# Optimization experiments

Hardware: AMD Instinct MI355X
Metric: run time of the kernel (lower is better)

The kernel has to match this reference:

```python
import jax, jax.numpy as jnp
import numpy as np

HIDDEN = 768
NUM_HEADS = 12
HEAD_DIM = HIDDEN // NUM_HEADS  # 64


def setup_inputs() -> dict:
    key = jax.random.key(0)
    ks = jax.random.split(key, 7)
    B, S = 2, 4096
    scale = 1.0 / np.sqrt(HIDDEN)
    return {
        "hidden_states": jax.random.normal(ks[0], (B, S, HIDDEN), dtype=jnp.float32),
        "Wq": jax.random.normal(ks[1], (HIDDEN, HIDDEN), dtype=jnp.float32) * scale,
        "bq": jnp.zeros((HIDDEN,), dtype=jnp.float32),
        "Wk": jax.random.normal(ks[2], (HIDDEN, HIDDEN), dtype=jnp.float32) * scale,
        "bk": jnp.zeros((HIDDEN,), dtype=jnp.float32),
        "Wv": jax.random.normal(ks[3], (HIDDEN, HIDDEN), dtype=jnp.float32) * scale,
        "bv": jnp.zeros((HIDDEN,), dtype=jnp.float32),
    }


def _split_heads(x):
    # [B, S, H] -> [B, heads, S, head_dim]
    B, S, _ = x.shape
    return x.reshape(B, S, NUM_HEADS, HEAD_DIM).transpose(0, 2, 1, 3)


def reference(hidden_states, Wq, bq, Wk, bk, Wv, bv):
    q = _split_heads(hidden_states @ Wq + bq)  # [B, h, S, d]
    k = _split_heads(hidden_states @ Wk + bk)
    v = _split_heads(hidden_states @ Wv + bv)
    scores = jnp.einsum("bhqd,bhkd->bhqk", q, k) / np.sqrt(HEAD_DIM)
    probs = jax.nn.softmax(scores, axis=-1)  # [B, h, S, S] materialized (eager attn)
    ctx = jnp.einsum("bhqk,bhkd->bhqd", probs, v)
    B, _, S, _ = ctx.shape
    return ctx.transpose(0, 2, 1, 3).reshape(B, S, HIDDEN)
```

## Files before the change

kernel.cpp:

```cpp
#include <hip/hip_runtime.h>
#include <hip/hip_bf16.h>

typedef unsigned short ushort_t;
typedef __attribute__((ext_vector_type(4))) float f32x4;
typedef __attribute__((ext_vector_type(8))) __bf16 bfrag;

#define MFMA16(a,b,c) __builtin_amdgcn_mfma_f32_16x16x32_bf16((a),(b),(c),0,0,0)

#define HID 768
#define NH 12
#define SEQ 4096
#define QSCALE 0.18033688011112042f

#define WAIT_VMCNT0() asm volatile("s_waitcnt vmcnt(0)" ::: "memory")

__device__ __forceinline__ unsigned short f2bf(float x) {
  union { float f; unsigned u; } v; v.f = x;
  unsigned r = v.u + 0x7fffu + ((v.u >> 16) & 1u);
  return (unsigned short)(r >> 16);
}

typedef const unsigned char __attribute__((address_space(1)))* gas1_t;
typedef unsigned char __attribute__((address_space(3)))* las3_t;
__device__ __forceinline__ void gload_lds16(const void* g, void* l) {
  __builtin_amdgcn_global_load_lds((gas1_t)(unsigned long long)g,
                                   (las3_t)(unsigned)(unsigned long long)l,
                                   16, 0, 0);
}

__device__ __forceinline__ f32x4 zero4() { f32x4 z = {0.f, 0.f, 0.f, 0.f}; return z; }

__global__ __launch_bounds__(256) void cvt_hidden(const float* __restrict__ hs,
                                                  ushort_t* __restrict__ A) {
  int i = blockIdx.x * 256 + threadIdx.x;
  float4 v = ((const float4*)hs)[i];
  ushort4 o;
  o.x = f2bf(v.x); o.y = f2bf(v.y); o.z = f2bf(v.z); o.w = f2bf(v.w);
  ((ushort4*)A)[i] = o;
}

__global__ __launch_bounds__(256) void transpose_w(const float* __restrict__ Wq,
                                                   const float* __restrict__ Wk,
                                                   const float* __restrict__ Wv,
                                                   ushort_t* __restrict__ Wt) {
  const int z = blockIdx.z;
  const float* W = (z == 0) ? Wq : ((z == 1) ? Wk : Wv);
  const int k0 = blockIdx.x * 64, n0 = blockIdx.y * 64;
  __shared__ float tile[64][65];
  const int t = threadIdx.x;
  const int c4 = (t & 15) * 4;
  const int r = t >> 4;
#pragma unroll
  for (int it = 0; it < 4; ++it) {
    int rr = r + it * 16;
    float4 v = *(const float4*)&W[(size_t)(k0 + rr) * HID + n0 + c4];
    tile[c4 + 0][rr] = v.x; tile[c4 + 1][rr] = v.y;
    tile[c4 + 2][rr] = v.z; tile[c4 + 3][rr] = v.w;
  }
  __syncthreads();
#pragma unroll
  for (int it = 0; it < 4; ++it) {
    int nl = r + it * 16;
    ushort4 o;
    o.x = f2bf(tile[nl][c4 + 0]); o.y = f2bf(tile[nl][c4 + 1]);
    o.z = f2bf(tile[nl][c4 + 2]); o.w = f2bf(tile[nl][c4 + 3]);
    *(ushort4*)&Wt[((size_t)z * HID + n0 + nl) * HID + k0 + c4] = o;
  }
}

__global__ __launch_bounds__(256) void qkv_gemm(const ushort_t* __restrict__ A,
                                                const ushort_t* __restrict__ Wt,
                                                const float* __restrict__ bq,
                                                const float* __restrict__ bk,
                                                const float* __restrict__ bv,
                                                ushort_t* __restrict__ Qh,
                                                ushort_t* __restrict__ Kh,
                                                ushort_t* __restrict__ Vt) {
  __shared__ ushort_t Als[128 * 64];
  __shared__ ushort_t Bls[128 * 64];
  const int z = blockIdx.z;
  const int m0 = blockIdx.x * 128, n0 = blockIdx.y * 128;
  const ushort_t* Wz = Wt + (size_t)z * HID * HID;
  const float* bias = (z == 0) ? bq : ((z == 1) ? bk : bv);
  const int t = threadIdx.x, w = t >> 6, lane = t & 63;
  const int g = lane >> 4, qc = lane & 15;
  const int srow = lane >> 3, sch = lane & 7;
  const int wm = w >> 1, wn = w & 1;

  f32x4 acc[4][4];
#pragma unroll
  for (int mt = 0; mt < 4; ++mt)
#pragma unroll
    for (int nt = 0; nt < 4; ++nt) acc[mt][nt] = zero4();

  for (int kt = 0; kt < 12; ++kt) {
    const int k0 = kt * 64;
#pragma unroll
    for (int i = 0; i < 4; ++i) {
      int row = w * 32 + i * 8 + srow;
      int chA = sch ^ (srow & 7);
      gload_lds16(&A[(size_t)(m0 + row) * HID + k0 + chA * 8],
                  &Als[(w * 32 + i * 8) * 64]);
      gload_lds16(&Wz[(size_t)(n0 + row) * HID + k0 + chA * 8],
                  &Bls[(w * 32 + i * 8) * 64]);
    }
    WAIT_VMCNT0();
    __syncthreads();
#pragma unroll
    for (int kk = 0; kk < 2; ++kk) {
      bfrag af[4], bf_[4];
#pragma unroll
      for (int mt = 0; mt < 4; ++mt) {
        int row = wm * 64 + mt * 16 + qc;
        af[mt] = *(const bfrag*)((const char*)Als + row * 128 +
                                 (((kk * 4 + g) ^ (qc & 7)) << 4));
      }
#pragma unroll
      for (int nt = 0; nt < 4; ++nt) {
        int row = wn * 64 + nt * 16 + qc;
        bf_[nt] = *(const bfrag*)((const char*)Bls + row * 128 +
                                  (((kk * 4 + g) ^ (qc & 7)) << 4));
      }
#pragma unroll
      for (int mt = 0; mt < 4; ++mt)
#pragma unroll
        for (int nt = 0; nt < 4; ++nt)
          acc[mt][nt] = MFMA16(af[mt], bf_[nt], acc[mt][nt]);
    }
    __syncthreads();
  }

#pragma unroll
  for (int mt = 0; mt < 4; ++mt) {
#pragma unroll
    for (int nt = 0; nt < 4; ++nt) {
      int n = n0 + wn * 64 + nt * 16 + qc;
      int head = n >> 6, d = n & 63;
      float bb = bias[n];
      int mB = m0 + wm * 64 + mt * 16 + 4 * g;
      int bidx = mB >> 12, s0 = mB & 4095;
      f32x4 a = acc[mt][nt];
      if (z == 2) {
        ushort4 o;
        o.x = f2bf(a[0] + bb); o.y = f2bf(a[1] + bb);
        o.z = f2bf(a[2] + bb); o.w = f2bf(a[3] + bb);
        int scol = (s0 & ~31) | (((s0 >> 2) & 3) << 3) | (((s0 >> 4) & 1) << 2);
        *(ushort4*)&Vt[((size_t)((bidx * NH + head) * 64 + d)) * SEQ + scol] = o;
      } else {
        ushort_t* dst = (z == 0) ? Qh : Kh;
        float sc = (z == 0) ? QSCALE : 1.0f;
        size_t base = (size_t)(bidx * NH + head) * SEQ;
#pragma unroll
        for (int i = 0; i < 4; ++i)
          dst[(base + s0 + i) * 64 + d] = f2bf((a[i] + bb) * sc);
      }
    }
  }
}

__device__ __forceinline__ void stage_tile(const ushort_t* __restrict__ Kb,
                                           const ushort_t* __restrict__ Vb,
                                           ushort_t* Kd, ushort_t* Vd,
                                           int kb, const int* jr, const int* jc, int w) {
#pragma unroll
  for (int i = 0; i < 2; ++i) {
    gload_lds16(&Kb[(size_t)(kb + jr[i]) * 64 + jc[i] * 8], &Kd[(w * 128 + i * 64) * 8]);
    gload_lds16(&Vb[(size_t)jr[i] * SEQ + kb + jc[i] * 8], &Vd[(w * 128 + i * 64) * 8]);
  }
}

__device__ __forceinline__ void tile_compute(const ushort_t* Kc, const ushort_t* Vc,
                                             const bfrag (&qv)[2][2],
                                             f32x4 (&o)[2][4], f32x4 (&lacc)[2],
                                             bfrag ones, int g, int qc) {
  bfrag ak[4][2];
#pragma unroll
  for (int s = 0; s < 4; ++s) {
    const int r = s * 16 + qc;
    ak[s][0] = *(const bfrag*)&Kc[r * 64 + ((g ^ (qc & 7)) * 8)];
    ak[s][1] = *(const bfrag*)&Kc[r * 64 + (((4 + g) ^ (qc & 7)) * 8)];
  }
  f32x4 st0[4], st1[4];
#pragma unroll
  for (int s = 0; s < 4; ++s) {
    f32x4 z = zero4();
    z = MFMA16(ak[s][0], qv[0][0], z);
    st0[s] = MFMA16(ak[s][1], qv[0][1], z);
  }
#pragma unroll
  for (int s = 0; s < 4; ++s) {
    f32x4 z = zero4();
    z = MFMA16(ak[s][0], qv[1][0], z);
    st1[s] = MFMA16(ak[s][1], qv[1][1], z);
  }
  bfrag bp0[2], bp1[2];
#pragma unroll
  for (int i = 0; i < 4; ++i) {
    bp0[0][i]     = (__bf16)__builtin_amdgcn_exp2f(st0[0][i]);
    bp0[0][4 + i] = (__bf16)__builtin_amdgcn_exp2f(st0[1][i]);
    bp0[1][i]     = (__bf16)__builtin_amdgcn_exp2f(st0[2][i]);
    bp0[1][4 + i] = (__bf16)__builtin_amdgcn_exp2f(st0[3][i]);
  }
  lacc[0] = MFMA16(ones, bp0[0], lacc[0]);
  lacc[0] = MFMA16(ones, bp0[1], lacc[0]);
#pragma unroll
  for (int i = 0; i < 4; ++i) {
    bp1[0][i]     = (__bf16)__builtin_amdgcn_exp2f(st1[0][i]);
    bp1[0][4 + i] = (__bf16)__builtin_amdgcn_exp2f(st1[1][i]);
    bp1[1][i]     = (__bf16)__builtin_amdgcn_exp2f(st1[2][i]);
    bp1[1][4 + i] = (__bf16)__builtin_amdgcn_exp2f(st1[3][i]);
  }
  lacc[1] = MFMA16(ones, bp1[0], lacc[1]);
  lacc[1] = MFMA16(ones, bp1[1], lacc[1]);
#pragma unroll
  for (int kk = 0; kk < 2; ++kk) {
#pragma unroll
    for (int dt = 0; dt < 4; ++dt) {
      bfrag av = *(const bfrag*)&Vc[(dt * 16 + qc) * 64 + (((kk * 4 + g) ^ (qc & 7)) * 8)];
      o[0][dt] = MFMA16(av, bp0[kk], o[0][dt]);
      o[1][dt] = MFMA16(av, bp1[kk], o[1][dt]);
    }
  }
}

__global__ __launch_bounds__(256, 3) void attn_kernel(const ushort_t* __restrict__ Qh,
                                                      const ushort_t* __restrict__ Kh,
                                                      const ushort_t* __restrict__ Vt,
                                                      float* __restrict__ out) {
  const int bh = blockIdx.y;
  const int b = bh / NH, head = bh - b * NH;
  const int t = threadIdx.x, w = t >> 6, lane = t & 63;
  const int g = lane >> 4, qc = lane & 15;
  const ushort_t* Qb = Qh + (size_t)bh * SEQ * 64;
  const ushort_t* Kb = Kh + (size_t)bh * SEQ * 64;
  const ushort_t* Vb = Vt + (size_t)bh * 64 * SEQ;
  const int q0 = blockIdx.x * 128 + w * 32;

  __shared__ ushort_t Kls[2][4096];
  __shared__ ushort_t Vls[2][4096];

  int jr[2], jc[2];
#pragma unroll
  for (int i = 0; i < 2; ++i) {
    int j = w * 128 + i * 64 + lane;
    jr[i] = j >> 3;
    jc[i] = (j & 7) ^ (jr[i] & 7);
  }

  bfrag qv[2][2];
#pragma unroll
  for (int qf = 0; qf < 2; ++qf)
#pragma unroll
    for (int dd = 0; dd < 2; ++dd)
      qv[qf][dd] = *(const bfrag*)&Qb[(size_t)(q0 + qf * 16 + qc) * 64 + dd * 32 + g * 8];

  f32x4 o[2][4];
  f32x4 lacc[2];
#pragma unroll
  for (int qf = 0; qf < 2; ++qf) {
    lacc[qf] = zero4();
#pragma unroll
    for (int dt = 0; dt < 4; ++dt) o[qf][dt] = zero4();
  }
  bfrag ones;
#pragma unroll
  for (int j = 0; j < 8; ++j) ones[j] = (__bf16)1.0f;

  stage_tile(Kb, Vb, &Kls[0][0], &Vls[0][0], 0, jr, jc, w);

  for (int kt2 = 0; kt2 < 32; ++kt2) {
    const int k0 = kt2 * 2;
    WAIT_VMCNT0();
    __syncthreads();
    stage_tile(Kb, Vb, &Kls[1][0], &Vls[1][0], (k0 + 1) * 64, jr, jc, w);
    tile_compute(&Kls[0][0], &Vls[0][0], qv, o, lacc, ones, g, qc);
    WAIT_VMCNT0();
    __syncthreads();
    if (kt2 < 31)
      stage_tile(Kb, Vb, &Kls[0][0], &Vls[0][0], (k0 + 2) * 64, jr, jc, w);
    tile_compute(&Kls[1][0], &Vls[1][0], qv, o, lacc, ones, g, qc);
  }

#pragma unroll
  for (int qf = 0; qf < 2; ++qf) {
    float inv = 1.0f / lacc[qf][0];
    int qrow = q0 + qf * 16 + qc;
    float* orow = out + (size_t)(b * SEQ + qrow) * HID + head * 64;
#pragma unroll
    for (int dt = 0; dt < 4; ++dt) {
      float4 vv;
      vv.x = o[qf][dt][0] * inv; vv.y = o[qf][dt][1] * inv;
      vv.z = o[qf][dt][2] * inv; vv.w = o[qf][dt][3] * inv;
      *(float4*)(orow + dt * 16 + 4 * g) = vv;
    }
  }
}

extern "C" void kernel_launch(void* const* d_in, const int* in_sizes, int n_in,
                              void* d_out, int out_size, void* d_ws, size_t ws_size,
                              hipStream_t stream) {
  (void)in_sizes; (void)n_in; (void)out_size; (void)ws_size;
  const float* hs = (const float*)d_in[0];
  const float* Wq = (const float*)d_in[1];
  const float* bq = (const float*)d_in[2];
  const float* Wk = (const float*)d_in[3];
  const float* bk = (const float*)d_in[4];
  const float* Wv = (const float*)d_in[5];
  const float* bv = (const float*)d_in[6];
  float* out = (float*)d_out;

  char* ws = (char*)d_ws;
  ushort_t* Abf = (ushort_t*)ws;
  ushort_t* Wt  = (ushort_t*)(ws + 12582912);
  ushort_t* Qh  = (ushort_t*)(ws + 12582912 + 3538944);
  ushort_t* Kh  = Qh + 6291456;
  ushort_t* Vt  = Kh + 6291456;

  cvt_hidden<<<6144, 256, 0, stream>>>(hs, Abf);
  transpose_w<<<dim3(12, 12, 3), 256, 0, stream>>>(Wq, Wk, Wv, Wt);
  qkv_gemm<<<dim3(64, 6, 3), 256, 0, stream>>>(Abf, Wt, bq, bk, bv, Qh, Kh, Vt);
  attn_kernel<<<dim3(32, 24), 256, 0, stream>>>(Qh, Kh, Vt, out);
}
```

Before: 165.2 us.

## Software-pipeline QK of next tile with softmax/PV of current, triple-buffer LDS

Splits the per-tile attention compute into a QK score stage and a softmax-plus-PV stage. The QK product for tile k+1 is issued alongside the exp and PV work for tile k, so MFMA and exp/VALU work can interleave. K/V LDS buffering goes from double to triple, with a loop unrolled by three and a tail PV step. This is meant to hide MFMA and exp latency within a wave. In exchange it keeps two sets of score registers live and uses 48KB of LDS per block, which may cost occupancy at 3 blocks per CU or cause spills.

```diff
diff --git a/kernel.cpp b/kernel.cpp
--- a/kernel.cpp
+++ b/kernel.cpp
@@ -13,6 +13,7 @@
 #define QSCALE 0.18033688011112042f
 
 #define WAIT_VMCNT0() asm volatile("s_waitcnt vmcnt(0)" ::: "memory")
+#define WAIT_VMCNT4() asm volatile("s_waitcnt vmcnt(4)" ::: "memory")
 
 __device__ __forceinline__ unsigned short f2bf(float x) {
   union { float f; unsigned u; } v; v.f = x;
@@ -169,10 +170,8 @@
   }
 }
 
-__device__ __forceinline__ void tile_compute(const ushort_t* Kc, const ushort_t* Vc,
-                                             const bfrag (&qv)[2][2],
-                                             f32x4 (&o)[2][4], f32x4 (&lacc)[2],
-                                             bfrag ones, int g, int qc) {
+__device__ __forceinline__ void qk_tile(const ushort_t* Kc, const bfrag (&qv)[2][2],
+                                        f32x4 (&st)[2][4], int g, int qc) {
   bfrag ak[4][2];
 #pragma unroll
   for (int s = 0; s < 4; ++s) {
@@ -180,47 +179,40 @@
     ak[s][0] = *(const bfrag*)&Kc[r * 64 + ((g ^ (qc & 7)) * 8)];
     ak[s][1] = *(const bfrag*)&Kc[r * 64 + (((4 + g) ^ (qc & 7)) * 8)];
   }
-  f32x4 st0[4], st1[4];
-#pragma unroll
-  for (int s = 0; s < 4; ++s) {
-    f32x4 z = zero4();
-    z = MFMA16(ak[s][0], qv[0][0], z);
-    st0[s] = MFMA16(ak[s][1], qv[0][1], z);
-  }
-#pragma unroll
-  for (int s = 0; s < 4; ++s) {
-    f32x4 z = zero4();
-    z = MFMA16(ak[s][0], qv[1][0], z);
-    st1[s] = MFMA16(ak[s][1], qv[1][1], z);
-  }
-  bfrag bp0[2], bp1[2];
-#pragma unroll
-  for (int i = 0; i < 4; ++i) {
-    bp0[0][i]     = (__bf16)__builtin_amdgcn_exp2f(st0[0][i]);
-    bp0[0][4 + i] = (__bf16)__builtin_amdgcn_exp2f(st0[1][i]);
-    bp0[1][i]     = (__bf16)__builtin_amdgcn_exp2f(st0[2][i]);
-    bp0[1][4 + i] = (__bf16)__builtin_amdgcn_exp2f(st0[3][i]);
-  }
-  lacc[0] = MFMA16(ones, bp0[0], lacc[0]);
-  lacc[0] = MFMA16(ones, bp0[1], lacc[0]);
-#pragma unroll
-  for (int i = 0; i < 4; ++i) {
-    bp1[0][i]     = (__bf16)__builtin_amdgcn_exp2f(st1[0][i]);
-    bp1[0][4 + i] = (__bf16)__builtin_amdgcn_exp2f(st1[1][i]);
-    bp1[1][i]     = (__bf16)__builtin_amdgcn_exp2f(st1[2][i]);
-    bp1[1][4 + i] = (__bf16)__builtin_amdgcn_exp2f(st1[3][i]);
-  }
-  lacc[1] = MFMA16(ones, bp1[0], lacc[1]);
-  lacc[1] = MFMA16(ones, bp1[1], lacc[1]);
-#pragma unroll
-  for (int kk = 0; kk < 2; ++kk) {
+#pragma unroll
+  for (int qf = 0; qf < 2; ++qf)
+#pragma unroll
+    for (int s = 0; s < 4; ++s) {
+      f32x4 z = zero4();
+      z = MFMA16(ak[s][0], qv[qf][0], z);
+      st[qf][s] = MFMA16(ak[s][1], qv[qf][1], z);
+    }
+}
+
+__device__ __forceinline__ void sm_pv_tile(const ushort_t* Vc, const f32x4 (&st)[2][4],
+                                           f32x4 (&o)[2][4], f32x4 (&lacc)[2],
+                                           bfrag ones, int g, int qc) {
+  bfrag bp[2][2];
+#pragma unroll
+  for (int qf = 0; qf < 2; ++qf) {
+#pragma unroll
+    for (int i = 0; i < 4; ++i) {
+      bp[qf][0][i]     = (__bf16)__builtin_amdgcn_exp2f(st[qf][0][i]);
+      bp[qf][0][4 + i] = (__bf16)__builtin_amdgcn_exp2f(st[qf][1][i]);
+      bp[qf][1][i]     = (__bf16)__builtin_amdgcn_exp2f(st[qf][2][i]);
+      bp[qf][1][4 + i] = (__bf16)__builtin_amdgcn_exp2f(st[qf][3][i]);
+    }
+    lacc[qf] = MFMA16(ones, bp[qf][0], lacc[qf]);
+    lacc[qf] = MFMA16(ones, bp[qf][1], lacc[qf]);
+  }
+#pragma unroll
+  for (int kk = 0; kk < 2; ++kk)
 #pragma unroll
     for (int dt = 0; dt < 4; ++dt) {
       bfrag av = *(const bfrag*)&Vc[(dt * 16 + qc) * 64 + (((kk * 4 + g) ^ (qc & 7)) * 8)];
-      o[0][dt] = MFMA16(av, bp0[kk], o[0][dt]);
-      o[1][dt] = MFMA16(av, bp1[kk], o[1][dt]);
-    }
-  }
+      o[0][dt] = MFMA16(av, bp[0][kk], o[0][dt]);
+      o[1][dt] = MFMA16(av, bp[1][kk], o[1][dt]);
+    }
 }
 
 __global__ __launch_bounds__(256, 3) void attn_kernel(const ushort_t* __restrict__ Qh,
@@ -236,8 +228,8 @@
   const ushort_t* Vb = Vt + (size_t)bh * 64 * SEQ;
   const int q0 = blockIdx.x * 128 + w * 32;
 
-  __shared__ ushort_t Kls[2][4096];
-  __shared__ ushort_t Vls[2][4096];
+  __shared__ ushort_t Kls[3][4096];
+  __shared__ ushort_t Vls[3][4096];
 
   int jr[2], jc[2];
 #pragma unroll
@@ -267,19 +259,37 @@
   for (int j = 0; j < 8; ++j) ones[j] = (__bf16)1.0f;
 
   stage_tile(Kb, Vb, &Kls[0][0], &Vls[0][0], 0, jr, jc, w);
-
-  for (int kt2 = 0; kt2 < 32; ++kt2) {
-    const int k0 = kt2 * 2;
+  stage_tile(Kb, Vb, &Kls[1][0], &Vls[1][0], 64, jr, jc, w);
+  f32x4 stA[2][4], stB[2][4];
+  WAIT_VMCNT4();
+  __syncthreads();
+  qk_tile(&Kls[0][0], qv, stA, g, qc);
+
+  for (int tt = 0; tt < 21; ++tt) {
+    const int t0 = tt * 3;
     WAIT_VMCNT0();
     __syncthreads();
-    stage_tile(Kb, Vb, &Kls[1][0], &Vls[1][0], (k0 + 1) * 64, jr, jc, w);
-    tile_compute(&Kls[0][0], &Vls[0][0], qv, o, lacc, ones, g, qc);
+    stage_tile(Kb, Vb, &Kls[2][0], &Vls[2][0], (t0 + 2) * 64, jr, jc, w);
+    qk_tile(&Kls[1][0], qv, stB, g, qc);
+    sm_pv_tile(&Vls[0][0], stA, o, lacc, ones, g, qc);
     WAIT_VMCNT0();
     __syncthreads();
-    if (kt2 < 31)
-      stage_tile(Kb, Vb, &Kls[0][0], &Vls[0][0], (k0 + 2) * 64, jr, jc, w);
-    tile_compute(&Kls[1][0], &Vls[1][0], qv, o, lacc, ones, g, qc);
-  }
+    stage_tile(Kb, Vb, &Kls[0][0], &Vls[0][0], (t0 + 3) * 64, jr, jc, w);
+    qk_tile(&Kls[2][0], qv, stA, g, qc);
+    sm_pv_tile(&Vls[1][0], stB, o, lacc, ones, g, qc);
+    WAIT_VMCNT0();
+    __syncthreads();
+    if (tt < 20)
+      stage_tile(Kb, Vb, &Kls[1][0], &Vls[1][0], (t0 + 4) * 64, jr, jc, w);
+    qk_tile(&Kls[0][0], qv, stB, g, qc);
+    sm_pv_tile(&Vls[2][0], stA, o, lacc, ones, g, qc);
+#pragma unroll
+    for (int qf = 0; qf < 2; ++qf)
+#pragma unroll
+      for (int s = 0; s < 4; ++s) stA[qf][s] = stB[qf][s];
+  }
+
+  sm_pv_tile(&Vls[0][0], stA, o, lacc, ones, g, qc);
 
 #pragma unroll
   for (int qf = 0; qf < 2; ++qf) {
```

New measurement: 166.6 us. About the same (+0.8%).
